# Kernel tuning notes

Measured on AMD Instinct MI355X. Metric: run time of the kernel, lower is better.

## Reference

```python
import jax, jax.numpy as jnp
import numpy as np

SOS_TOKEN = 0


def setup_inputs() -> dict:
    key = jax.random.key(0)
    ks = jax.random.split(key, 16)
    B, S, T, H, V = 64, 64, 32, 512, 32000
    s = 1.0 / np.sqrt(H)
    inp = {
        "encoder_outputs": jax.random.normal(ks[0], (B, S, H), jnp.float32),
        "encoder_hidden": jax.random.normal(ks[1], (1, B, H), jnp.float32),
        "target_tensor": jax.random.randint(ks[2], (B, T), 0, V),
        "emb": jax.random.normal(ks[3], (V, H), jnp.float32),
        "Wa": jax.random.uniform(ks[4], (H, H), jnp.float32, -s, s),
        "ba": jnp.zeros((H,), jnp.float32),
        "Ua": jax.random.uniform(ks[5], (H, H), jnp.float32, -s, s),
        "bu": jnp.zeros((H,), jnp.float32),
        "va": jax.random.uniform(ks[6], (H, 1), jnp.float32, -s, s),
        "bv": jnp.zeros((1,), jnp.float32),
        "w_ih": jax.random.uniform(ks[7], (3 * H, 2 * H), jnp.float32, -s, s),
        "b_ih": jax.random.uniform(ks[8], (3 * H,), jnp.float32, -s, s),
        "w_hh": jax.random.uniform(ks[9], (3 * H, H), jnp.float32, -s, s),
        "b_hh": jax.random.uniform(ks[10], (3 * H,), jnp.float32, -s, s),
        "Wo": jax.random.uniform(ks[11], (V, H), jnp.float32, -s, s),
        "bo": jax.random.uniform(ks[12], (V,), jnp.float32, -s, s),
    }
    return inp


def _gru_cell(x, h, w_ih, b_ih, w_hh, b_hh):
    # x: [B, 2H], h: [B, H] -- PyTorch nn.GRU gate math
    H = h.shape[-1]
    gi = x @ w_ih.T + b_ih            # [B, 3H]
    gh = h @ w_hh.T + b_hh            # [B, 3H]
    i_r, i_z, i_n = gi[:, :H], gi[:, H:2 * H], gi[:, 2 * H:]
    h_r, h_z, h_n = gh[:, :H], gh[:, H:2 * H], gh[:, 2 * H:]
    r = jax.nn.sigmoid(i_r + h_r)
    z = jax.nn.sigmoid(i_z + h_z)
    n = jnp.tanh(i_n + r * h_n)
    return (1.0 - z) * n + z * h


def reference(encoder_outputs, encoder_hidden, target_tensor,
              emb, Wa, ba, Ua, bu, va, bv,
              w_ih, b_ih, w_hh, b_hh, Wo, bo):
    B, S, H = encoder_outputs.shape
    T = target_tensor.shape[1]
    # Teacher forcing: step t input is SOS for t=0 else target[:, t-1]
    sos = jnp.full((B, 1), SOS_TOKEN, dtype=target_tensor.dtype)
    input_ids = jnp.concatenate([sos, target_tensor[:, :-1]], axis=1)  # [B, T]
    embedded = emb[input_ids]  # [B, T, H]  (dropout is identity in eval)

    # Precompute key projection once (invariant across steps)
    Ua_keys = encoder_outputs @ Ua.T + bu  # [B, S, H]

    def step(h, x_emb):
        # Bahdanau additive attention: query = hidden state
        scores = jnp.tanh(h[:, None, :] @ Wa.T + ba + Ua_keys) @ va + bv  # [B, S, 1]
        scores = scores[..., 0]                                           # [B, S]
        attn = jax.nn.softmax(scores, axis=-1)
        context = jnp.einsum('bs,bsh->bh', attn, encoder_outputs)
        x = jnp.concatenate([x_emb, context], axis=-1)                    # [B, 2H]
        h_new = _gru_cell(x, h, w_ih, b_ih, w_hh, b_hh)
        logits = h_new @ Wo.T + bo                                        # [B, V]
        return h_new, (logits, attn)

    h0 = encoder_hidden[0]  # [B, H]
    h_final, (logits_t, attn_t) = jax.lax.scan(step, h0, jnp.swapaxes(embedded, 0, 1))
    logits = jnp.swapaxes(logits_t, 0, 1)        # [B, T, V]
    attentions = jnp.swapaxes(attn_t, 0, 1)      # [B, T, S]
    log_probs = jax.nn.log_softmax(logits, axis=-1)
    decoder_hidden = h_final[None]               # [1, B, H]
    return (log_probs, decoder_hidden, attentions)
```

## Files before the change

### kernel.cpp

```cpp
#include <hip/hip_runtime.h>

typedef unsigned short u16;
typedef __bf16 bf16x8 __attribute__((ext_vector_type(8)));
typedef float f32x4 __attribute__((ext_vector_type(4)));

#define Bsz 64
#define Ssz 64
#define Tsz 32
#define Hsz 512
#define Vsz 32000
#define NBLK 96

static __device__ inline u16 f2bf(float f) {
    union { float f; unsigned u; } v; v.f = f;
    unsigned u = v.u;
    unsigned r = (u + 0x7FFFu + ((u >> 16) & 1u)) >> 16;
    return (u16)r;
}
static __device__ inline float bf2f(u16 v) {
    union { unsigned u; float f; } x; x.u = ((unsigned)v) << 16; return x.f;
}
static __device__ inline float tanh_fast(float x) {
    float e = __expf(2.f * x);
    return 1.f - 2.f / (e + 1.f);
}
static __device__ inline void st_f32(float* p, float v) {
    __hip_atomic_store(p, v, __ATOMIC_RELAXED, __HIP_MEMORY_SCOPE_AGENT);
}
static __device__ inline void st_u32(unsigned* p, unsigned v) {
    __hip_atomic_store(p, v, __ATOMIC_RELAXED, __HIP_MEMORY_SCOPE_AGENT);
}

#define GLOAD_LDS16(g, l) \
    __builtin_amdgcn_global_load_lds((const __attribute__((address_space(1))) void*)(g), \
                                     (__attribute__((address_space(3))) void*)(l), 16, 0, 0)

__global__ void prep_kernel(const float* __restrict__ enc, const float* __restrict__ Ua,
                            const float* __restrict__ Wa, const float* __restrict__ wih,
                            const float* __restrict__ whh, const float* __restrict__ Wo,
                            const float* __restrict__ ehid,
                            u16* __restrict__ encbf, u16* __restrict__ Uabf,
                            u16* __restrict__ Wabf, u16* __restrict__ wihbf,
                            u16* __restrict__ whhbf, u16* __restrict__ Wobf,
                            u16* __restrict__ h0bf) {
    const int n0 = 2097152, n1 = 262144, n2 = 262144, n3 = 1572864, n4 = 786432, n5 = 16384000, n6 = 32768;
    const int total = n0 + n1 + n2 + n3 + n4 + n5 + n6;
    for (int i = blockIdx.x * blockDim.x + threadIdx.x; i < total; i += gridDim.x * blockDim.x) {
        int j = i;
        if (j < n0) { encbf[j] = f2bf(enc[j]); continue; } j -= n0;
        if (j < n1) { Uabf[j] = f2bf(Ua[j]); continue; } j -= n1;
        if (j < n2) { Wabf[j] = f2bf(Wa[j]); continue; } j -= n2;
        if (j < n3) { wihbf[j] = f2bf(wih[j]); continue; } j -= n3;
        if (j < n4) { whhbf[j] = f2bf(whh[j]); continue; } j -= n4;
        if (j < n5) { Wobf[j] = f2bf(Wo[j]); continue; } j -= n5;
        h0bf[j] = f2bf(ehid[j]);
    }
}

__global__ void embed_kernel(const int* __restrict__ target, const float* __restrict__ emb,
                             u16* __restrict__ xbuf) {
    int n = Tsz * Bsz * Hsz;
    for (int i = blockIdx.x * blockDim.x + threadIdx.x; i < n; i += gridDim.x * blockDim.x) {
        int t = i / (Bsz * Hsz);
        int rem = i % (Bsz * Hsz);
        int b = rem / Hsz, k = rem % Hsz;
        int id = (t == 0) ? 0 : target[b * Tsz + (t - 1)];
        xbuf[((size_t)t * Bsz + b) * 1024 + k] = f2bf(emb[(size_t)id * Hsz + k]);
    }
}

template <int MODE>
__global__ __launch_bounds__(256) void gemm_bt(const u16* __restrict__ A, const u16* __restrict__ Bw,
                                               const float* __restrict__ bias, float* __restrict__ out,
                                               float* __restrict__ sumexp,
                                               int M, int N, int K) {
    __shared__ __align__(16) u16 As[128 * 32];
    __shared__ __align__(16) u16 Bs[128 * 32];
    int m0 = blockIdx.x * 128, n0 = blockIdx.y * 128;
    int tid = threadIdx.x, lane = tid & 63, wid = tid >> 6;
    int wm = wid & 1, wn = wid >> 1;
    f32x4 acc[4][4] = {};
    for (int k0 = 0; k0 < K; k0 += 32) {
        int e0 = wid * 64 + lane;
        int e1 = e0 + 256;
        GLOAD_LDS16(&A[(size_t)(m0 + (e0 >> 2)) * K + k0 + (e0 & 3) * 8], (char*)As + wid * 1024);
        GLOAD_LDS16(&A[(size_t)(m0 + (e1 >> 2)) * K + k0 + (e1 & 3) * 8], (char*)As + 4096 + wid * 1024);
        GLOAD_LDS16(&Bw[(size_t)(n0 + (e0 >> 2)) * K + k0 + (e0 & 3) * 8], (char*)Bs + wid * 1024);
        GLOAD_LDS16(&Bw[(size_t)(n0 + (e1 >> 2)) * K + k0 + (e1 & 3) * 8], (char*)Bs + 4096 + wid * 1024);
        __syncthreads();
        bf16x8 av[4], bvv[4];
        for (int mi = 0; mi < 4; ++mi)
            av[mi] = *(const bf16x8*)&As[(wm * 64 + mi * 16 + (lane & 15)) * 32 + (lane >> 4) * 8];
        for (int ni = 0; ni < 4; ++ni)
            bvv[ni] = *(const bf16x8*)&Bs[(wn * 64 + ni * 16 + (lane & 15)) * 32 + (lane >> 4) * 8];
        for (int mi = 0; mi < 4; ++mi)
            for (int ni = 0; ni < 4; ++ni)
                acc[mi][ni] = __builtin_amdgcn_mfma_f32_16x16x32_bf16(av[mi], bvv[ni], acc[mi][ni], 0, 0, 0);
        __syncthreads();
    }
    float rowpart[4][4];
    if (MODE == 1)
        for (int mi = 0; mi < 4; ++mi)
            for (int r = 0; r < 4; ++r) rowpart[mi][r] = 0.f;
    for (int mi = 0; mi < 4; ++mi)
        for (int ni = 0; ni < 4; ++ni) {
            int n = n0 + wn * 64 + ni * 16 + (lane & 15);
            float bb = bias[n];
            for (int r = 0; r < 4; ++r) {
                int m = m0 + wm * 64 + mi * 16 + (lane >> 4) * 4 + r;
                float val = acc[mi][ni][r] + bb;
                if (MODE == 0)
                    out[(size_t)m * N + n] = val;
                else {
                    int t = m >> 6, b = m & 63;
                    out[((size_t)(b * Tsz + t)) * Vsz + n] = val;
                    rowpart[mi][r] += __expf(val);
                }
            }
        }
    if (MODE == 1) {
        for (int mi = 0; mi < 4; ++mi)
            for (int r = 0; r < 4; ++r) {
                float v = rowpart[mi][r];
                v += __shfl_xor(v, 1);
                v += __shfl_xor(v, 2);
                v += __shfl_xor(v, 4);
                v += __shfl_xor(v, 8);
                if ((lane & 15) == 0) {
                    int m = m0 + wm * 64 + mi * 16 + (lane >> 4) * 4 + r;
                    int rowp = (m & 63) * Tsz + (m >> 6);
                    atomicAdd(&sumexp[rowp], v);
                }
            }
    }
}

static __device__ inline void arrive(unsigned* bar, int slot, unsigned val, int tid) {
    asm volatile("s_waitcnt vmcnt(0)" ::: "memory");
    __syncthreads();
    if (tid == 0) st_u32(&bar[slot * 32], val);
}
static __device__ inline void pollflags(unsigned* bar, int base, int n, unsigned target, int tid) {
    if (tid < n) {
        unsigned* p = &bar[(base + tid) * 32];
        while (__hip_atomic_load(p, __ATOMIC_RELAXED, __HIP_MEMORY_SCOPE_AGENT) < target) {}
    }
    __syncthreads();
}

__global__ __launch_bounds__(512, 1) void coop_kernel(
    const float* __restrict__ uak, float* __restrict__ Whbuf,
    u16* __restrict__ xbuf, u16* __restrict__ Abf,
    const u16* __restrict__ h0bf, const u16* __restrict__ wihbf, const u16* __restrict__ whhbf,
    const u16* __restrict__ Wabf, const float* __restrict__ enc,
    const float* __restrict__ va, const float* __restrict__ bv, const float* __restrict__ ba,
    const float* __restrict__ b_ih, const float* __restrict__ b_hh,
    const float* __restrict__ ehid, float* __restrict__ out,
    unsigned* __restrict__ bar) {
    __shared__ __align__(16) char lds[147456];
    __shared__ float WhL[512];
    __shared__ float scL[64];
    __shared__ float vaL[512];

    const size_t HID_OFF = (size_t)Bsz * Tsz * Vsz;
    const size_t ATT_OFF = HID_OFF + (size_t)Bsz * Hsz;

    int tid = threadIdx.x, lane = tid & 63, wid = tid >> 6;
    int ln15 = lane & 15, hi = lane >> 4;
    int bx = blockIdx.x;
    bool isB = bx < 64;
    int g = bx - 64, jbase = g * 16;

    unsigned* xbufU = (unsigned*)xbuf;
    unsigned* AbfU = (unsigned*)Abf;

    if (isB) {
        int b = bx;
        u16* uakL = (u16*)lds;
        u16* encL = (u16*)(lds + 65536);
        for (int i = tid; i < Ssz * Hsz; i += 512) {
            uakL[i] = f2bf(uak[(size_t)b * Ssz * Hsz + i]);
            encL[i] = f2bf(enc[(size_t)b * Ssz * Hsz + i]);
        }
        vaL[tid] = va[tid];
        float bvv = bv[0];
        __syncthreads();

        for (int t = 0; t < Tsz; ++t) {
            pollflags(bar, 64, 32, 3u * t + 1u, tid);
            WhL[tid] = Whbuf[(size_t)t * Bsz * Hsz + (size_t)b * 512 + tid];
            __syncthreads();
            for (int si = 0; si < 8; ++si) {
                int s = wid * 8 + si;
                float a = 0.f;
#pragma unroll
                for (int ji = 0; ji < 8; ++ji) {
                    int j = lane + ji * 64;
                    float x = WhL[j] + bf2f(uakL[s * 512 + j]);
                    a += tanh_fast(x) * vaL[j];
                }
                for (int off = 32; off; off >>= 1) a += __shfl_down(a, off);
                if (lane == 0) scL[s] = a + bvv;
            }
            __syncthreads();
            if (wid == 0) {
                float x = scL[lane];
                float mx = x;
                for (int off = 32; off; off >>= 1) mx = fmaxf(mx, __shfl_xor(mx, off));
                float e = __expf(x - mx);
                float sm = e;
                for (int off = 32; off; off >>= 1) sm += __shfl_xor(sm, off);
                float at = e / sm;
                scL[lane] = at;
                out[ATT_OFF + ((size_t)b * Tsz + t) * Ssz + lane] = at;
            }
            __syncthreads();
            float c = 0.f;
            for (int s = 0; s < Ssz; ++s)
                c += scL[s] * bf2f(encL[s * 512 + tid]);
            unsigned me = (unsigned)f2bf(c);
            unsigned other = __shfl_xor(me, 1);
            if ((tid & 1) == 0)
                st_u32(&xbufU[((size_t)t * Bsz + b) * 512 + 256 + (tid >> 1)], me | (other << 16));
            arrive(bar, bx, 3u * t + 2u, tid);
        }
    } else {
        for (int i = tid; i < 6144; i += 512) {
            int row = i >> 7, c16 = i & 127;
            int Rg = (row >> 4) * 512 + jbase + (row & 15);
            uint4 v = *(const uint4*)&wihbf[(size_t)Rg * 1024 + c16 * 8];
            *(uint4*)(lds + row * 2048 + ((c16 * 16) ^ ((row & 7) << 4))) = v;
        }
        for (int i = tid; i < 3072; i += 512) {
            int row = i >> 6, c16 = i & 63;
            int Rg = (row >> 4) * 512 + jbase + (row & 15);
            uint4 v = *(const uint4*)&whhbf[(size_t)Rg * 512 + c16 * 8];
            *(uint4*)(lds + 98304 + row * 1024 + ((c16 * 16) ^ ((row & 7) << 4))) = v;
        }
        const char* wih_l = lds;
        const char* whh_l = lds + 98304;
        int j = jbase + ln15;
        float ba_j = ba[j];
        float bir = b_ih[j] + b_hh[j];
        float biz = b_ih[512 + j] + b_hh[512 + j];
        float bin = b_ih[1024 + j];
        float bhn = b_hh[1024 + j];
        float hp0 = 0.f, hp1 = 0.f, hp2 = 0.f, hp3 = 0.f;
        if (wid < 4) {
            int m = wid;
            hp0 = ehid[(size_t)(m * 16 + hi * 4 + 0) * Hsz + j];
            hp1 = ehid[(size_t)(m * 16 + hi * 4 + 1) * Hsz + j];
            hp2 = ehid[(size_t)(m * 16 + hi * 4 + 2) * Hsz + j];
            hp3 = ehid[(size_t)(m * 16 + hi * 4 + 3) * Hsz + j];
        }
        int swz = (ln15 & 7) << 4;

        for (int t = 0; t < Tsz; ++t) {
            const u16* hbt = (t == 0) ? h0bf : (Abf + (size_t)(t - 1) * Bsz * Hsz);
            float* Whb = Whbuf + (size_t)t * Bsz * Hsz;
            pollflags(bar, 64, 32, 3u * t, tid);
            if (wid < 4) {
                int m = wid;
                f32x4 acc = {};
#pragma unroll
                for (int k0 = 0; k0 < 16; ++k0) {
                    bf16x8 a = *(const bf16x8*)&hbt[(size_t)(m * 16 + ln15) * 512 + k0 * 32 + hi * 8];
                    bf16x8 bw = *(const bf16x8*)&Wabf[(size_t)(jbase + ln15) * 512 + k0 * 32 + hi * 8];
                    acc = __builtin_amdgcn_mfma_f32_16x16x32_bf16(a, bw, acc, 0, 0, 0);
                }
#pragma unroll
                for (int r = 0; r < 4; ++r)
                    st_f32(&Whb[(size_t)(m * 16 + hi * 4 + r) * 512 + j], acc[r] + ba_j);
            }
            arrive(bar, bx, 3u * t + 1u, tid);
            f32x4 ar = {}, az = {}, ain = {}, ahn = {};
            if (wid < 4) {
                int m = wid;
#pragma unroll 8
                for (int k0 = 0; k0 < 16; ++k0) {
                    bf16x8 a = *(const bf16x8*)&xbuf[((size_t)t * Bsz + m * 16 + ln15) * 1024 + k0 * 32 + hi * 8];
                    int byteIn = k0 * 64 + hi * 16;
                    bf16x8 b0 = *(const bf16x8*)(wih_l + (0 + ln15) * 2048 + (byteIn ^ swz));
                    bf16x8 b1 = *(const bf16x8*)(wih_l + (16 + ln15) * 2048 + (byteIn ^ swz));
                    bf16x8 b2 = *(const bf16x8*)(wih_l + (32 + ln15) * 2048 + (byteIn ^ swz));
                    ar = __builtin_amdgcn_mfma_f32_16x16x32_bf16(a, b0, ar, 0, 0, 0);
                    az = __builtin_amdgcn_mfma_f32_16x16x32_bf16(a, b1, az, 0, 0, 0);
                    ain = __builtin_amdgcn_mfma_f32_16x16x32_bf16(a, b2, ain, 0, 0, 0);
                }
#pragma unroll 8
                for (int k0 = 0; k0 < 16; ++k0) {
                    bf16x8 a = *(const bf16x8*)&hbt[(size_t)(m * 16 + ln15) * 512 + k0 * 32 + hi * 8];
                    int byteIn = k0 * 64 + hi * 16;
                    bf16x8 b0 = *(const bf16x8*)(whh_l + (0 + ln15) * 1024 + (byteIn ^ swz));
                    bf16x8 b1 = *(const bf16x8*)(whh_l + (16 + ln15) * 1024 + (byteIn ^ swz));
                    bf16x8 b2 = *(const bf16x8*)(whh_l + (32 + ln15) * 1024 + (byteIn ^ swz));
                    ar = __builtin_amdgcn_mfma_f32_16x16x32_bf16(a, b0, ar, 0, 0, 0);
                    az = __builtin_amdgcn_mfma_f32_16x16x32_bf16(a, b1, az, 0, 0, 0);
                    ahn = __builtin_amdgcn_mfma_f32_16x16x32_bf16(a, b2, ahn, 0, 0, 0);
                }
            }
            pollflags(bar, 0, 64, 3u * t + 2u, tid);
            if (wid < 4) {
                int m = wid;
#pragma unroll 8
                for (int k0 = 16; k0 < 32; ++k0) {
                    bf16x8 a = *(const bf16x8*)&xbuf[((size_t)t * Bsz + m * 16 + ln15) * 1024 + k0 * 32 + hi * 8];
                    int byteIn = k0 * 64 + hi * 16;
                    bf16x8 b0 = *(const bf16x8*)(wih_l + (0 + ln15) * 2048 + (byteIn ^ swz));
                    bf16x8 b1 = *(const bf16x8*)(wih_l + (16 + ln15) * 2048 + (byteIn ^ swz));
                    bf16x8 b2 = *(const bf16x8*)(wih_l + (32 + ln15) * 2048 + (byteIn ^ swz));
                    ar = __builtin_amdgcn_mfma_f32_16x16x32_bf16(a, b0, ar, 0, 0, 0);
                    az = __builtin_amdgcn_mfma_f32_16x16x32_bf16(a, b1, az, 0, 0, 0);
                    ain = __builtin_amdgcn_mfma_f32_16x16x32_bf16(a, b2, ain, 0, 0, 0);
                }
                float hpv[4] = {hp0, hp1, hp2, hp3};
#pragma unroll
                for (int r = 0; r < 4; ++r) {
                    int b = m * 16 + hi * 4 + r;
                    float rg = 1.f / (1.f + __expf(-(ar[r] + bir)));
                    float zg = 1.f / (1.f + __expf(-(az[r] + biz)));
                    float ng = tanh_fast(ain[r] + bin + rg * (ahn[r] + bhn));
                    float hv = (1.f - zg) * ng + zg * hpv[r];
                    hpv[r] = hv;
                    unsigned me = (unsigned)f2bf(hv);
                    unsigned other = __shfl_xor(me, 1);
                    if ((ln15 & 1) == 0)
                        st_u32(&AbfU[((size_t)t * Bsz + b) * 256 + (j >> 1)], me | (other << 16));
                    if (t == Tsz - 1) out[HID_OFF + (size_t)b * 512 + j] = hv;
                }
                hp0 = hpv[0]; hp1 = hpv[1]; hp2 = hpv[2]; hp3 = hpv[3];
            }
            arrive(bar, bx, 3u * t + 3u, tid);
        }
    }
}

__global__ void sub_kernel(float* __restrict__ out, const float* __restrict__ sumexp) {
    const int total4 = (Bsz * Tsz * Vsz) / 4;
    float4* o4 = (float4*)out;
    for (int i = blockIdx.x * blockDim.x + threadIdx.x; i < total4; i += gridDim.x * blockDim.x) {
        float l = __logf(sumexp[i / (Vsz / 4)]);
        float4 v = o4[i];
        v.x -= l; v.y -= l; v.z -= l; v.w -= l;
        o4[i] = v;
    }
}

extern "C" void kernel_launch(void* const* d_in, const int* in_sizes, int n_in,
                              void* d_out, int out_size, void* d_ws, size_t ws_size,
                              hipStream_t stream) {
    const float* enc   = (const float*)d_in[0];
    const float* ehid  = (const float*)d_in[1];
    const int*   target= (const int*)d_in[2];
    const float* emb   = (const float*)d_in[3];
    const float* Wa    = (const float*)d_in[4];
    const float* ba    = (const float*)d_in[5];
    const float* Ua    = (const float*)d_in[6];
    const float* bu    = (const float*)d_in[7];
    const float* va    = (const float*)d_in[8];
    const float* bv    = (const float*)d_in[9];
    const float* w_ih  = (const float*)d_in[10];
    const float* b_ih  = (const float*)d_in[11];
    const float* w_hh  = (const float*)d_in[12];
    const float* b_hh  = (const float*)d_in[13];
    const float* Wo    = (const float*)d_in[14];
    const float* bo    = (const float*)d_in[15];
    float* out = (float*)d_out;

    char* w = (char*)d_ws;
    float* uak   = (float*)w; w += (size_t)4096 * 512 * 4;
    float* Whbuf = (float*)w; w += (size_t)Tsz * Bsz * Hsz * 4;
    float* sumexp= (float*)w; w += 8192;
    unsigned* bar= (unsigned*)w; w += 96 * 128;
    u16* xbuf    = (u16*)w;   w += (size_t)Tsz * Bsz * 1024 * 2;
    u16* Abf     = (u16*)w;   w += (size_t)Tsz * Bsz * Hsz * 2;
    u16* h0bf    = (u16*)w;   w += (size_t)Bsz * Hsz * 2;
    u16* Wabf    = (u16*)w;   w += (size_t)Hsz * Hsz * 2;
    u16* encbf   = (u16*)w;   w += (size_t)4096 * 512 * 2;
    u16* Uabf    = (u16*)w;   w += (size_t)Hsz * Hsz * 2;
    u16* wihbf   = (u16*)w;   w += (size_t)1536 * 1024 * 2;
    u16* whhbf   = (u16*)w;   w += (size_t)1536 * 512 * 2;
    u16* Wobf    = (u16*)w;   w += (size_t)Vsz * 512 * 2;

    prep_kernel<<<2048, 256, 0, stream>>>(enc, Ua, Wa, w_ih, w_hh, Wo, ehid,
                                          encbf, Uabf, Wabf, wihbf, whhbf, Wobf, h0bf);
    embed_kernel<<<1024, 256, 0, stream>>>(target, emb, xbuf);

    gemm_bt<0><<<dim3(32, 4), 256, 0, stream>>>(encbf, Uabf, bu, uak, (float*)nullptr, 4096, 512, 512);

    hipMemsetAsync(bar, 0, 96 * 128, stream);
    hipMemsetAsync(sumexp, 0, 2048 * 4, stream);

    coop_kernel<<<NBLK, 512, 0, stream>>>(uak, Whbuf, xbuf, Abf, h0bf, wihbf, whhbf,
                                          Wabf, enc, va, bv, ba, b_ih, b_hh, ehid, out, bar);

    gemm_bt<1><<<dim3(16, 250), 256, 0, stream>>>(Abf, Wobf, bo, out, sumexp, 2048, Vsz, 512);

    sub_kernel<<<2048, 256, 0, stream>>>(out, sumexp);
}
```

Measured before the change: 969.3 us.

## Overlap output-projection GEMM with recurrent decoder via extra persistent blocks

Moves the vocabulary-projection GEMM plus its sum-exp reduction into the persistent cooperative kernel. 160 extra blocks poll the GRU-completion flags and process 4-timestep chunks while the recurrence keeps running. The goal is to hide the large logits GEMM behind the latency-bound sequential decoder and drop one kernel launch. The GRU blocks' poll on attention flags is also narrowed to per-wave loads without a block barrier. Risks: 256 blocks of 512 threads with large LDS must all be co-resident or the spin-waits deadlock, and the GEMM blocks may steal bandwidth from the critical path.

```diff
diff --git a/kernel.cpp b/kernel.cpp
--- a/kernel.cpp
+++ b/kernel.cpp
@@ -10,6 +10,8 @@
 #define Hsz 512
 #define Vsz 32000
 #define NBLK 96
+#define NLBLK 160
+#define NTOT 256
 
 static __device__ inline u16 f2bf(float f) {
     union { float f; unsigned u; } v; v.f = f;
@@ -69,10 +71,8 @@
     }
 }
 
-template <int MODE>
 __global__ __launch_bounds__(256) void gemm_bt(const u16* __restrict__ A, const u16* __restrict__ Bw,
                                                const float* __restrict__ bias, float* __restrict__ out,
-                                               float* __restrict__ sumexp,
                                                int M, int N, int K) {
     __shared__ __align__(16) u16 As[128 * 32];
     __shared__ __align__(16) u16 Bs[128 * 32];
@@ -98,41 +98,15 @@
                 acc[mi][ni] = __builtin_amdgcn_mfma_f32_16x16x32_bf16(av[mi], bvv[ni], acc[mi][ni], 0, 0, 0);
         __syncthreads();
     }
-    float rowpart[4][4];
-    if (MODE == 1)
-        for (int mi = 0; mi < 4; ++mi)
-            for (int r = 0; r < 4; ++r) rowpart[mi][r] = 0.f;
     for (int mi = 0; mi < 4; ++mi)
         for (int ni = 0; ni < 4; ++ni) {
             int n = n0 + wn * 64 + ni * 16 + (lane & 15);
             float bb = bias[n];
             for (int r = 0; r < 4; ++r) {
                 int m = m0 + wm * 64 + mi * 16 + (lane >> 4) * 4 + r;
-                float val = acc[mi][ni][r] + bb;
-                if (MODE == 0)
-                    out[(size_t)m * N + n] = val;
-                else {
-                    int t = m >> 6, b = m & 63;
-                    out[((size_t)(b * Tsz + t)) * Vsz + n] = val;
-                    rowpart[mi][r] += __expf(val);
-                }
-            }
-        }
-    if (MODE == 1) {
-        for (int mi = 0; mi < 4; ++mi)
-            for (int r = 0; r < 4; ++r) {
-                float v = rowpart[mi][r];
-                v += __shfl_xor(v, 1);
-                v += __shfl_xor(v, 2);
-                v += __shfl_xor(v, 4);
-                v += __shfl_xor(v, 8);
-                if ((lane & 15) == 0) {
-                    int m = m0 + wm * 64 + mi * 16 + (lane >> 4) * 4 + r;
-                    int rowp = (m & 63) * Tsz + (m >> 6);
-                    atomicAdd(&sumexp[rowp], v);
-                }
-            }
-    }
+                out[(size_t)m * N + n] = acc[mi][ni][r] + bb;
+            }
+        }
 }
 
 static __device__ inline void arrive(unsigned* bar, int slot, unsigned val, int tid) {
@@ -152,10 +126,11 @@
     const float* __restrict__ uak, float* __restrict__ Whbuf,
     u16* __restrict__ xbuf, u16* __restrict__ Abf,
     const u16* __restrict__ h0bf, const u16* __restrict__ wihbf, const u16* __restrict__ whhbf,
-    const u16* __restrict__ Wabf, const float* __restrict__ enc,
+    const u16* __restrict__ Wabf, const u16* __restrict__ Wobf,
+    const float* __restrict__ enc,
     const float* __restrict__ va, const float* __restrict__ bv, const float* __restrict__ ba,
-    const float* __restrict__ b_ih, const float* __restrict__ b_hh,
-    const float* __restrict__ ehid, float* __restrict__ out,
+    const float* __restrict__ b_ih, const float* __restrict__ b_hh, const float* __restrict__ bo,
+    const float* __restrict__ ehid, float* __restrict__ out, float* __restrict__ sumexp,
     unsigned* __restrict__ bar) {
     __shared__ __align__(16) char lds[147456];
     __shared__ float WhL[512];
@@ -168,13 +143,11 @@
     int tid = threadIdx.x, lane = tid & 63, wid = tid >> 6;
     int ln15 = lane & 15, hi = lane >> 4;
     int bx = blockIdx.x;
-    bool isB = bx < 64;
-    int g = bx - 64, jbase = g * 16;
 
     unsigned* xbufU = (unsigned*)xbuf;
     unsigned* AbfU = (unsigned*)Abf;
 
-    if (isB) {
+    if (bx < 64) {
         int b = bx;
         u16* uakL = (u16*)lds;
         u16* encL = (u16*)(lds + 65536);
@@ -224,7 +197,8 @@
                 st_u32(&xbufU[((size_t)t * Bsz + b) * 512 + 256 + (tid >> 1)], me | (other << 16));
             arrive(bar, bx, 3u * t + 2u, tid);
         }
-    } else {
+    } else if (bx < 96) {
+        int jbase = (bx - 64) * 16;
         for (int i = tid; i < 6144; i += 512) {
             int row = i >> 7, c16 = i & 127;
             int Rg = (row >> 4) * 512 + jbase + (row & 15);
@@ -299,7 +273,10 @@
                     ahn = __builtin_amdgcn_mfma_f32_16x16x32_bf16(a, b2, ahn, 0, 0, 0);
                 }
             }
-            pollflags(bar, 0, 64, 3u * t + 2u, tid);
+            if (wid < 4) {
+                unsigned* p = &bar[(wid * 16 + ln15) * 32];
+                while (__hip_atomic_load(p, __ATOMIC_RELAXED, __HIP_MEMORY_SCOPE_AGENT) < 3u * t + 2u) {}
+            }
             if (wid < 4) {
                 int m = wid;
 #pragma unroll 8
@@ -331,6 +308,64 @@
                 hp0 = hpv[0]; hp1 = hpv[1]; hp2 = hpv[2]; hp3 = hpv[3];
             }
             arrive(bar, bx, 3u * t + 3u, tid);
+        }
+    } else {
+        int lb = bx - 96;
+        u16* As = (u16*)lds;
+        u16* Bs = (u16*)(lds + 8192);
+        int wm = wid & 1, wn = wid >> 1;
+        int polled_c = -1;
+        for (int job = lb; job < 4000; job += NLBLK) {
+            int c = job / 500, idx = job % 500;
+            int mt = idx / 250, nt = idx % 250;
+            if (c != polled_c) {
+                pollflags(bar, 64, 32, 12u * c + 12u, tid);
+                polled_c = c;
+            }
+            int m0 = c * 256 + mt * 128, n0 = nt * 128;
+            f32x4 acc[4][2] = {};
+            for (int k0 = 0; k0 < 512; k0 += 32) {
+                int r = tid >> 2, c8 = (tid & 3) * 8;
+                GLOAD_LDS16(&Abf[(size_t)(m0 + r) * 512 + k0 + c8], (char*)As + wid * 1024);
+                GLOAD_LDS16(&Wobf[(size_t)(n0 + r) * 512 + k0 + c8], (char*)Bs + wid * 1024);
+                __syncthreads();
+                bf16x8 av[4], bvv[2];
+                for (int mi = 0; mi < 4; ++mi)
+                    av[mi] = *(const bf16x8*)&As[(wm * 64 + mi * 16 + ln15) * 32 + hi * 8];
+                for (int ni = 0; ni < 2; ++ni)
+                    bvv[ni] = *(const bf16x8*)&Bs[(wn * 32 + ni * 16 + ln15) * 32 + hi * 8];
+                for (int mi = 0; mi < 4; ++mi)
+                    for (int ni = 0; ni < 2; ++ni)
+                        acc[mi][ni] = __builtin_amdgcn_mfma_f32_16x16x32_bf16(av[mi], bvv[ni], acc[mi][ni], 0, 0, 0);
+                __syncthreads();
+            }
+            float rowpart[4][4];
+            for (int mi = 0; mi < 4; ++mi)
+                for (int r = 0; r < 4; ++r) rowpart[mi][r] = 0.f;
+            for (int mi = 0; mi < 4; ++mi)
+                for (int ni = 0; ni < 2; ++ni) {
+                    int n = n0 + wn * 32 + ni * 16 + ln15;
+                    float bb = bo[n];
+                    for (int r = 0; r < 4; ++r) {
+                        int m = m0 + wm * 64 + mi * 16 + hi * 4 + r;
+                        int t = m >> 6, b = m & 63;
+                        float val = acc[mi][ni][r] + bb;
+                        out[((size_t)(b * Tsz + t)) * Vsz + n] = val;
+                        rowpart[mi][r] += __expf(val);
+                    }
+                }
+            for (int mi = 0; mi < 4; ++mi)
+                for (int r = 0; r < 4; ++r) {
+                    float v = rowpart[mi][r];
+                    v += __shfl_xor(v, 1);
+                    v += __shfl_xor(v, 2);
+                    v += __shfl_xor(v, 4);
+                    v += __shfl_xor(v, 8);
+                    if (ln15 == 0) {
+                        int m = m0 + wm * 64 + mi * 16 + hi * 4 + r;
+                        atomicAdd(&sumexp[(m & 63) * Tsz + (m >> 6)], v);
+                    }
+                }
         }
     }
 }
@@ -386,15 +421,14 @@
                                           encbf, Uabf, Wabf, wihbf, whhbf, Wobf, h0bf);
     embed_kernel<<<1024, 256, 0, stream>>>(target, emb, xbuf);
 
-    gemm_bt<0><<<dim3(32, 4), 256, 0, stream>>>(encbf, Uabf, bu, uak, (float*)nullptr, 4096, 512, 512);
+    gemm_bt<<<dim3(32, 4), 256, 0, stream>>>(encbf, Uabf, bu, uak, 4096, 512, 512);
 
     hipMemsetAsync(bar, 0, 96 * 128, stream);
     hipMemsetAsync(sumexp, 0, 2048 * 4, stream);
 
-    coop_kernel<<<NBLK, 512, 0, stream>>>(uak, Whbuf, xbuf, Abf, h0bf, wihbf, whhbf,
-                                          Wabf, enc, va, bv, ba, b_ih, b_hh, ehid, out, bar);
-
-    gemm_bt<1><<<dim3(16, 250), 256, 0, stream>>>(Abf, Wobf, bo, out, sumexp, 2048, Vsz, 512);
+    coop_kernel<<<NTOT, 512, 0, stream>>>(uak, Whbuf, xbuf, Abf, h0bf, wihbf, whhbf,
+                                          Wabf, Wobf, enc, va, bv, ba, b_ih, b_hh, bo,
+                                          ehid, out, sumexp, bar);
 
     sub_kernel<<<2048, 256, 0, stream>>>(out, sumexp);
 }
```

New measurement: 1.061 ms. 1.09x slower.
